# Kernel optimization log

Hardware: AMD Instinct MI355X
Metric: run time of the kernel (lower is better)

The kernel has to match this reference:

```python
import math
import jax, jax.numpy as jnp
import numpy as np

K_NEIGH = 8  # module's self.k

def setup_inputs() -> dict:
    key = jax.random.key(0)
    ks = jax.random.split(key, 5)
    B, N, D = 4, 4096, 256
    s = 1.0 / math.sqrt(D)
    return {
        "x": jax.random.normal(ks[0], (B, N, D), dtype=jnp.float32),
        "Wqkv": jax.random.normal(ks[1], (3 * D, D), dtype=jnp.float32) * s,
        "bqkv": jax.random.normal(ks[2], (3 * D,), dtype=jnp.float32) * 0.02,
        "Wout": jax.random.normal(ks[3], (D, D), dtype=jnp.float32) * s,
        "bout": jax.random.normal(ks[4], (D,), dtype=jnp.float32) * 0.02,
    }

def reference(x, Wqkv, bqkv, Wout, bout):
    B, N, D = x.shape
    qkv = x @ Wqkv.T + bqkv                      # [B,N,3D]
    q, k, v = jnp.split(qkv, 3, axis=-1)         # each [B,N,D]
    # F.normalize(k, dim=-1) with eps=1e-12
    kn = k / jnp.maximum(jnp.linalg.norm(k, axis=-1, keepdims=True), 1e-12)
    sim = jnp.einsum('bnd,bmd->bnm', kn, kn)     # [B,N,N] cosine similarity
    sim = sim - 1e9 * jnp.eye(N, dtype=sim.dtype)
    k_val = min(K_NEIGH, N - 1)
    _, idx = jax.lax.top_k(sim, k_val)           # [B,N,k] neighbor indices
    # NOTE: the torch code builds k.unsqueeze(2).expand(B,N,N,D) and gathers on
    # dim 2, but that tensor is CONSTANT along dim 2, so the gather reduces to a
    # broadcast of k (and v) over the neighbor axis -- reproduced faithfully:
    k_sel = jnp.broadcast_to(k[:, :, None, :], (B, N, k_val, D))
    v_sel = jnp.broadcast_to(v[:, :, None, :], (B, N, k_val, D))
    scores = jnp.sum(q[:, :, None, :] * k_sel, axis=-1) / math.sqrt(D)  # [B,N,k]
    attn = jax.nn.softmax(scores, axis=-1)
    out = jnp.sum(attn[..., None] * v_sel, axis=2)                      # [B,N,D]
    return x + out @ Wout.T + bout
```

## Files before the change

### kernel.cpp

```cpp
#include <hip/hip_runtime.h>
#include <hip/hip_bf16.h>

#define DD 256
#define NROWS 16384

typedef float f32x4 __attribute__((ext_vector_type(4)));
typedef __bf16 bf16x4 __attribute__((ext_vector_type(4)));
typedef __bf16 bf16x8 __attribute__((ext_vector_type(8)));

__device__ __forceinline__ bf16x8 cvt8(f32x4 lo, f32x4 hi) {
  bf16x8 v;
#pragma unroll
  for (int j = 0; j < 4; ++j) {
    v[j] = (__bf16)lo[j];
    v[4 + j] = (__bf16)hi[j];
  }
  return v;
}

__global__ __launch_bounds__(1024) void wc_bc_kernel(
    const float* __restrict__ Wqkv, const float* __restrict__ bqkv,
    const float* __restrict__ Wout, const float* __restrict__ bout,
    __bf16* __restrict__ Wc, float* __restrict__ bc) {
  __shared__ f32x4 part[16][64];
  __shared__ float red[4];
  const int i = blockIdx.x;
  const int t = threadIdx.x;
  const int w = t >> 6, l = t & 63;
  const float* __restrict__ Wv = Wqkv + 2 * DD * DD;
  const float* __restrict__ bv = bqkv + 2 * DD;
  const float* __restrict__ wrow = Wout + (size_t)i * DD;

  f32x4 wr[4];
#pragma unroll
  for (int k = 0; k < 4; ++k) wr[k] = *(const f32x4*)(wrow + w * 16 + k * 4);

  const float* wvp = Wv + (size_t)(w * 16) * DD + l * 4;
  f32x4 a0 = {0.f, 0.f, 0.f, 0.f}, a1 = {0.f, 0.f, 0.f, 0.f};
  f32x4 a2 = {0.f, 0.f, 0.f, 0.f}, a3 = {0.f, 0.f, 0.f, 0.f};
#pragma unroll
  for (int k = 0; k < 4; ++k) {
    a0 += wr[k][0] * *(const f32x4*)(wvp + (size_t)(4 * k + 0) * DD);
    a1 += wr[k][1] * *(const f32x4*)(wvp + (size_t)(4 * k + 1) * DD);
    a2 += wr[k][2] * *(const f32x4*)(wvp + (size_t)(4 * k + 2) * DD);
    a3 += wr[k][3] * *(const f32x4*)(wvp + (size_t)(4 * k + 3) * DD);
  }
  part[w][l] = (a0 + a1) + (a2 + a3);

  if (t < 256) {
    float p = wrow[t] * bv[t];
#pragma unroll
    for (int off = 32; off > 0; off >>= 1) p += __shfl_down(p, off);
    if (l == 0) red[w] = p;
  }
  __syncthreads();
  if (w == 0) {
    f32x4 s = {0.f, 0.f, 0.f, 0.f};
#pragma unroll
    for (int k = 0; k < 16; ++k) s += part[k][l];
    bf16x4 o;
#pragma unroll
    for (int j = 0; j < 4; ++j) o[j] = (__bf16)s[j];
    *(bf16x4*)(Wc + (size_t)i * DD + l * 4) = o;
    if (l == 0) bc[i] = bout[i] + red[0] + red[1] + red[2] + red[3];
  }
}

__global__ __launch_bounds__(512, 4) void knn_attn_main(
    const float* __restrict__ x, const __bf16* __restrict__ Wc,
    const float* __restrict__ bc, float* __restrict__ out) {
  __shared__ __bf16 xs[32 * DD];

  const int t = threadIdx.x;
  const int w = t >> 6, l = t & 63;
  const int Rbase = blockIdx.x * 32;

  const int xrow = l & 15, g4 = l >> 4;
  const int rsw = (xrow & 7) << 4;

  bf16x8 af[2][8];
  f32x4 bias[2];
#pragma unroll
  for (int ct = 0; ct < 2; ++ct) {
    const __bf16* wrp = Wc + (size_t)(w * 32 + ct * 16 + xrow) * DD + g4 * 8;
#pragma unroll
    for (int ks = 0; ks < 8; ++ks) af[ct][ks] = *(const bf16x8*)(wrp + ks * 32);
    bias[ct] = *(const f32x4*)(bc + w * 32 + ct * 16 + g4 * 4);
  }

  {
    const int sr = t >> 4, sc = t & 15;
    const int ssw = (sr & 7) << 4;
    const int sbase = sr * 512 + sc * 32;
    const float* s0 = x + (size_t)(Rbase + sr) * DD + sc * 16;
    f32x4 a = *(const f32x4*)(s0 + 0);
    f32x4 b = *(const f32x4*)(s0 + 4);
    f32x4 c = *(const f32x4*)(s0 + 8);
    f32x4 d = *(const f32x4*)(s0 + 12);
    *(bf16x8*)((char*)xs + ((sbase + 0) ^ ssw)) = cvt8(a, b);
    *(bf16x8*)((char*)xs + ((sbase + 16) ^ ssw)) = cvt8(c, d);
  }
  __syncthreads();

#pragma unroll
  for (int i = 0; i < 2; ++i) {
    const int lrow = i * 16 + xrow;
    bf16x8 xf[8];
#pragma unroll
    for (int ks = 0; ks < 8; ++ks)
      xf[ks] = *(const bf16x8*)((const char*)xs +
                                ((lrow * 512 + ks * 64 + g4 * 16) ^ rsw));

#pragma unroll
    for (int ct = 0; ct < 2; ++ct) {
      f32x4 acc = {0.f, 0.f, 0.f, 0.f};
#pragma unroll
      for (int ks = 0; ks < 8; ++ks)
        acc = __builtin_amdgcn_mfma_f32_16x16x32_bf16(af[ct][ks], xf[ks], acc, 0, 0, 0);
      const int ocol = w * 32 + ct * 16 + g4 * 4;
      bf16x4 xr4 = *(const bf16x4*)((const char*)xs +
                                    ((lrow * 512 + ocol * 2) ^ rsw));
      f32x4 xres;
#pragma unroll
      for (int j = 0; j < 4; ++j) xres[j] = (float)xr4[j];
      *(f32x4*)(out + (size_t)(Rbase + i * 16 + xrow) * DD + ocol) =
          acc + xres + bias[ct];
    }
  }
}

extern "C" void kernel_launch(void* const* d_in, const int* in_sizes, int n_in,
                              void* d_out, int out_size, void* d_ws, size_t ws_size,
                              hipStream_t stream) {
  const float* x = (const float*)d_in[0];
  const float* Wqkv = (const float*)d_in[1];
  const float* bqkv = (const float*)d_in[2];
  const float* Wout = (const float*)d_in[3];
  const float* bout = (const float*)d_in[4];
  float* out = (float*)d_out;

  __bf16* Wc = (__bf16*)d_ws;
  float* bc = (float*)((char*)d_ws + DD * DD * sizeof(__bf16));

  wc_bc_kernel<<<DD, 1024, 0, stream>>>(Wqkv, bqkv, Wout, bout, Wc, bc);
  knn_attn_main<<<NROWS / 32, 512, 0, stream>>>(x, Wc, bc, out);
}
```

Measured before the change: 22.43 us.

## Fuse weight folding into main kernel as two chained per-block MFMA GEMMs

Drops the separate kernel that precomputed the folded weight Wout·Wv and bias. Instead, one kernel runs x@Wv^T+bv into a shared-memory bf16 tile, then multiplies that tile by Wout^T and adds the residual and bias. Each block now converts fp32 Wv and Wout slices to bf16 on the fly, and the row tile grows to 64 rows with 1024 threads. This removes one launch and the serial dependency between the two kernels. In exchange it doubles the matrix work, makes every block re-read both weight matrices from cache, and adds a second bf16 rounding of the intermediate.

Result: slower. 27.08 us (+20.7%).

```diff
diff --git a/kernel.cpp b/kernel.cpp
--- a/kernel.cpp
+++ b/kernel.cpp
@@ -3,6 +3,7 @@
 
 #define DD 256
 #define NROWS 16384
+#define BR 64
 
 typedef float f32x4 __attribute__((ext_vector_type(4)));
 typedef __bf16 bf16x4 __attribute__((ext_vector_type(4)));
@@ -18,74 +19,32 @@
   return v;
 }
 
-__global__ __launch_bounds__(1024) void wc_bc_kernel(
-    const float* __restrict__ Wqkv, const float* __restrict__ bqkv,
-    const float* __restrict__ Wout, const float* __restrict__ bout,
-    __bf16* __restrict__ Wc, float* __restrict__ bc) {
-  __shared__ f32x4 part[16][64];
-  __shared__ float red[4];
-  const int i = blockIdx.x;
-  const int t = threadIdx.x;
-  const int w = t >> 6, l = t & 63;
-  const float* __restrict__ Wv = Wqkv + 2 * DD * DD;
-  const float* __restrict__ bv = bqkv + 2 * DD;
-  const float* __restrict__ wrow = Wout + (size_t)i * DD;
-
-  f32x4 wr[4];
-#pragma unroll
-  for (int k = 0; k < 4; ++k) wr[k] = *(const f32x4*)(wrow + w * 16 + k * 4);
-
-  const float* wvp = Wv + (size_t)(w * 16) * DD + l * 4;
-  f32x4 a0 = {0.f, 0.f, 0.f, 0.f}, a1 = {0.f, 0.f, 0.f, 0.f};
-  f32x4 a2 = {0.f, 0.f, 0.f, 0.f}, a3 = {0.f, 0.f, 0.f, 0.f};
-#pragma unroll
-  for (int k = 0; k < 4; ++k) {
-    a0 += wr[k][0] * *(const f32x4*)(wvp + (size_t)(4 * k + 0) * DD);
-    a1 += wr[k][1] * *(const f32x4*)(wvp + (size_t)(4 * k + 1) * DD);
-    a2 += wr[k][2] * *(const f32x4*)(wvp + (size_t)(4 * k + 2) * DD);
-    a3 += wr[k][3] * *(const f32x4*)(wvp + (size_t)(4 * k + 3) * DD);
-  }
-  part[w][l] = (a0 + a1) + (a2 + a3);
-
-  if (t < 256) {
-    float p = wrow[t] * bv[t];
-#pragma unroll
-    for (int off = 32; off > 0; off >>= 1) p += __shfl_down(p, off);
-    if (l == 0) red[w] = p;
-  }
-  __syncthreads();
-  if (w == 0) {
-    f32x4 s = {0.f, 0.f, 0.f, 0.f};
-#pragma unroll
-    for (int k = 0; k < 16; ++k) s += part[k][l];
-    bf16x4 o;
-#pragma unroll
-    for (int j = 0; j < 4; ++j) o[j] = (__bf16)s[j];
-    *(bf16x4*)(Wc + (size_t)i * DD + l * 4) = o;
-    if (l == 0) bc[i] = bout[i] + red[0] + red[1] + red[2] + red[3];
-  }
-}
-
-__global__ __launch_bounds__(512, 4) void knn_attn_main(
-    const float* __restrict__ x, const __bf16* __restrict__ Wc,
-    const float* __restrict__ bc, float* __restrict__ out) {
-  __shared__ __bf16 xs[32 * DD];
+__global__ __launch_bounds__(1024, 4) void fused_knn(
+    const float* __restrict__ x, const float* __restrict__ Wqkv,
+    const float* __restrict__ bqkv, const float* __restrict__ Wout,
+    const float* __restrict__ bout, float* __restrict__ out) {
+  __shared__ __bf16 xs[BR * DD];
+  __shared__ __bf16 ts[BR * DD];
 
   const int t = threadIdx.x;
   const int w = t >> 6, l = t & 63;
-  const int Rbase = blockIdx.x * 32;
+  const int Rbase = blockIdx.x * BR;
+  const int xrow = l & 15, g4 = l >> 4;
+  const int C0 = w * 16;
 
-  const int xrow = l & 15, g4 = l >> 4;
-  const int rsw = (xrow & 7) << 4;
+  const float* __restrict__ Wv = Wqkv + 2 * DD * DD;
+  const float* __restrict__ bv = bqkv + 2 * DD;
 
-  bf16x8 af[2][8];
-  f32x4 bias[2];
+  const f32x4 bv4 = *(const f32x4*)(bv + C0 + g4 * 4);
+  const f32x4 bo4 = *(const f32x4*)(bout + C0 + g4 * 4);
+
+  bf16x8 af[8];
+  {
+    const float* wvr = Wv + (size_t)(C0 + xrow) * DD + g4 * 8;
 #pragma unroll
-  for (int ct = 0; ct < 2; ++ct) {
-    const __bf16* wrp = Wc + (size_t)(w * 32 + ct * 16 + xrow) * DD + g4 * 8;
-#pragma unroll
-    for (int ks = 0; ks < 8; ++ks) af[ct][ks] = *(const bf16x8*)(wrp + ks * 32);
-    bias[ct] = *(const f32x4*)(bc + w * 32 + ct * 16 + g4 * 4);
+    for (int ks = 0; ks < 8; ++ks)
+      af[ks] = cvt8(*(const f32x4*)(wvr + ks * 32),
+                    *(const f32x4*)(wvr + ks * 32 + 4));
   }
 
   {
@@ -103,29 +62,54 @@
   __syncthreads();
 
 #pragma unroll
-  for (int i = 0; i < 2; ++i) {
-    const int lrow = i * 16 + xrow;
+  for (int rt = 0; rt < 4; ++rt) {
+    const int lrow = rt * 16 + xrow;
+    const int lsw = (lrow & 7) << 4;
     bf16x8 xf[8];
 #pragma unroll
     for (int ks = 0; ks < 8; ++ks)
       xf[ks] = *(const bf16x8*)((const char*)xs +
-                                ((lrow * 512 + ks * 64 + g4 * 16) ^ rsw));
+                                ((lrow * 512 + ks * 64 + g4 * 16) ^ lsw));
+    f32x4 acc = {0.f, 0.f, 0.f, 0.f};
+#pragma unroll
+    for (int ks = 0; ks < 8; ++ks)
+      acc = __builtin_amdgcn_mfma_f32_16x16x32_bf16(af[ks], xf[ks], acc, 0, 0, 0);
+    acc += bv4;
+    bf16x4 tq;
+#pragma unroll
+    for (int j = 0; j < 4; ++j) tq[j] = (__bf16)acc[j];
+    *(bf16x4*)((char*)ts + ((lrow * 512 + (C0 + g4 * 4) * 2) ^ lsw)) = tq;
+  }
+
+  {
+    const float* wor = Wout + (size_t)(C0 + xrow) * DD + g4 * 8;
+#pragma unroll
+    for (int ks = 0; ks < 8; ++ks)
+      af[ks] = cvt8(*(const f32x4*)(wor + ks * 32),
+                    *(const f32x4*)(wor + ks * 32 + 4));
+  }
+  __syncthreads();
 
 #pragma unroll
-    for (int ct = 0; ct < 2; ++ct) {
-      f32x4 acc = {0.f, 0.f, 0.f, 0.f};
+  for (int rt = 0; rt < 4; ++rt) {
+    const int lrow = rt * 16 + xrow;
+    const int lsw = (lrow & 7) << 4;
+    bf16x8 tf[8];
 #pragma unroll
-      for (int ks = 0; ks < 8; ++ks)
-        acc = __builtin_amdgcn_mfma_f32_16x16x32_bf16(af[ct][ks], xf[ks], acc, 0, 0, 0);
-      const int ocol = w * 32 + ct * 16 + g4 * 4;
-      bf16x4 xr4 = *(const bf16x4*)((const char*)xs +
-                                    ((lrow * 512 + ocol * 2) ^ rsw));
-      f32x4 xres;
+    for (int ks = 0; ks < 8; ++ks)
+      tf[ks] = *(const bf16x8*)((const char*)ts +
+                                ((lrow * 512 + ks * 64 + g4 * 16) ^ lsw));
+    f32x4 acc = {0.f, 0.f, 0.f, 0.f};
 #pragma unroll
-      for (int j = 0; j < 4; ++j) xres[j] = (float)xr4[j];
-      *(f32x4*)(out + (size_t)(Rbase + i * 16 + xrow) * DD + ocol) =
-          acc + xres + bias[ct];
-    }
+    for (int ks = 0; ks < 8; ++ks)
+      acc = __builtin_amdgcn_mfma_f32_16x16x32_bf16(af[ks], tf[ks], acc, 0, 0, 0);
+    const int ocol = C0 + g4 * 4;
+    bf16x4 xr4 = *(const bf16x4*)((const char*)xs +
+                                  ((lrow * 512 + ocol * 2) ^ lsw));
+    f32x4 xres;
+#pragma unroll
+    for (int j = 0; j < 4; ++j) xres[j] = (float)xr4[j];
+    *(f32x4*)(out + (size_t)(Rbase + lrow) * DD + ocol) = acc + xres + bo4;
   }
 }
 
@@ -139,9 +123,5 @@
   const float* bout = (const float*)d_in[4];
   float* out = (float*)d_out;
 
-  __bf16* Wc = (__bf16*)d_ws;
-  float* bc = (float*)((char*)d_ws + DD * DD * sizeof(__bf16));
-
-  wc_bc_kernel<<<DD, 1024, 0, stream>>>(Wqkv, bqkv, Wout, bout, Wc, bc);
-  knn_attn_main<<<NROWS / 32, 512, 0, stream>>>(x, Wc, bc, out);
+  fused_knn<<<NROWS / BR, 1024, 0, stream>>>(x, Wqkv, bqkv, Wout, bout, out);
 }
```
